# Optimization experiments

Hardware: AMD Instinct MI355X
Metric: run time of the kernel (lower is better)

Reference implementation:

```python
import jax, jax.numpy as jnp
import numpy as np

NUM_HEADS = 8
KEY_DIM = 512      # total projected dim across heads
VALUE_DIM = 512
EMBED_DIM = 512


def setup_inputs() -> dict:
    key = jax.random.key(0)
    ks = jax.random.split(key, 12)
    B, S, E = 8, 1024, EMBED_DIM
    sc_in = 1.0 / np.sqrt(E)
    sc_o = 1.0 / np.sqrt(KEY_DIM)
    return {
        "queries": jax.random.normal(ks[0], (B, S, E), jnp.float32),
        "keys": jax.random.normal(ks[1], (B, S, E), jnp.float32),
        "values": jax.random.normal(ks[2], (B, S, E), jnp.float32),
        "Wq": jax.random.normal(ks[3], (E, KEY_DIM), jnp.float32) * sc_in,
        "bq": jnp.zeros((KEY_DIM,), jnp.float32),
        "Wk": jax.random.normal(ks[4], (E, KEY_DIM), jnp.float32) * sc_in,
        "bk": jnp.zeros((KEY_DIM,), jnp.float32),
        "Wv": jax.random.normal(ks[5], (E, VALUE_DIM), jnp.float32) * sc_in,
        "bv": jnp.zeros((VALUE_DIM,), jnp.float32),
        "Wo": jax.random.normal(ks[6], (KEY_DIM, EMBED_DIM), jnp.float32) * sc_o,
        "bo": jnp.zeros((EMBED_DIM,), jnp.float32),
    }


def _split_heads(x):
    # [B, S, key_dim] -> [B, H, S, key_dim//H]
    B, S, D = x.shape
    return x.reshape(B, S, NUM_HEADS, D // NUM_HEADS).transpose(0, 2, 1, 3)


def reference(queries, keys, values, Wq, bq, Wk, bk, Wv, bv, Wo, bo):
    q = _split_heads(queries @ Wq + bq)   # [B,H,S,dh]
    k = _split_heads(keys @ Wk + bk)
    v = _split_heads(values @ Wv + bv)
    # NOTE: original scales by sqrt(full key_dim), not per-head dim
    scores = jnp.einsum("bhqd,bhkd->bhqk", q, k) / jnp.sqrt(
        jnp.asarray(KEY_DIM, jnp.float32))
    weights = jax.nn.softmax(scores, axis=-1)
    o = jnp.einsum("bhqk,bhkd->bhqd", weights, v)  # [B,H,S,dh]
    B, H, S, dh = o.shape
    o = o.transpose(0, 2, 1, 3).reshape(B, S, H * dh)  # merge heads -> key_dim
    return o @ Wo + bo
```

## Files before the change

### kernel.cpp

```cpp
#include <hip/hip_runtime.h>


typedef __bf16 bf16x8 __attribute__((ext_vector_type(8)));
typedef __bf16 bf16x4 __attribute__((ext_vector_type(4)));
typedef float  f32x4  __attribute__((ext_vector_type(4)));

#define MFMA(a, b, c) __builtin_amdgcn_mfma_f32_16x16x32_bf16((a), (b), (c), 0, 0, 0)

__device__ inline bf16x8 cvt8(const float* p) {
  f32x4 u = *(const f32x4*)p;
  f32x4 v = *(const f32x4*)(p + 4);
  bf16x8 r;
  r[0] = (__bf16)u[0]; r[1] = (__bf16)u[1]; r[2] = (__bf16)u[2]; r[3] = (__bf16)u[3];
  r[4] = (__bf16)v[0]; r[5] = (__bf16)v[1]; r[6] = (__bf16)v[2]; r[7] = (__bf16)v[3];
  return r;
}

__device__ inline void gl_lds(const __bf16* g, __bf16* l) {
  __builtin_amdgcn_global_load_lds((const __attribute__((address_space(1))) void*)g,
                                   (__attribute__((address_space(3))) void*)l, 16, 0, 0);
}

__global__ __launch_bounds__(256) void cvt_qkv(const float* __restrict__ Q,
                                               const float* __restrict__ K,
                                               const float* __restrict__ V,
                                               __bf16* __restrict__ Qo,
                                               __bf16* __restrict__ Ko,
                                               __bf16* __restrict__ Vo) {
  const float* src;
  __bf16* dst;
  switch (blockIdx.y) {
    case 0: src = Q; dst = Qo; break;
    case 1: src = K; dst = Ko; break;
    default: src = V; dst = Vo; break;
  }
  const long idx = ((long)blockIdx.x * 256 + threadIdx.x) * 8;
  *(bf16x8*)(dst + idx) = cvt8(src + idx);
}

__global__ __launch_bounds__(256) void transpose_w4(const float* __restrict__ W0,
                                                    const float* __restrict__ W1,
                                                    const float* __restrict__ W2,
                                                    const float* __restrict__ W3,
                                                    __bf16* __restrict__ O0,
                                                    __bf16* __restrict__ O1,
                                                    __bf16* __restrict__ O2,
                                                    __bf16* __restrict__ O3,
                                                    float s0) {
  const float* in;
  __bf16* out;
  float sc = 1.0f;
  switch (blockIdx.y) {
    case 0: in = W0; out = O0; sc = s0; break;
    case 1: in = W1; out = O1; break;
    case 2: in = W2; out = O2; break;
    default: in = W3; out = O3; break;
  }
  __shared__ __align__(16) float t[64][65];
  const int tk = (blockIdx.x & 7) * 64;
  const int tn = (blockIdx.x >> 3) * 64;
  const int r0 = threadIdx.x >> 4;
  const int c4 = threadIdx.x & 15;
#pragma unroll
  for (int i = 0; i < 4; ++i) {
    int r = r0 + i * 16;
    f32x4 v = *(const f32x4*)(in + (long)(tk + r) * 512 + tn + c4 * 4);
#pragma unroll
    for (int j = 0; j < 4; ++j) t[r][c4 * 4 + j] = v[j] * sc;
  }
  __syncthreads();
  const int n0 = threadIdx.x >> 3;
  const int k8 = threadIdx.x & 7;
#pragma unroll
  for (int i = 0; i < 2; ++i) {
    int n = n0 + i * 32;
    bf16x8 v;
#pragma unroll
    for (int j = 0; j < 8; ++j) v[j] = (__bf16)t[k8 * 8 + j][n];
    *(bf16x8*)(out + (long)(tn + n) * 512 + tk + k8 * 8) = v;
  }
}

template <int MODE, typename OT>
__device__ __forceinline__ void gemm_core(const __bf16* __restrict__ X,
                                          const __bf16* __restrict__ Wt,
                                          const float* __restrict__ bias,
                                          OT* __restrict__ out, float bsc,
                                          char* smem) {
  __bf16 (*At)[4096] = (__bf16(*)[4096])smem;
  __bf16 (*Bt)[4096] = (__bf16(*)[4096])(smem + 16384);

  const int tid = threadIdx.x;
  const int lane = tid & 63, wid = tid >> 6, quad = lane >> 4, l16 = lane & 15;
  const int i = blockIdx.x;
  const int kk = i >> 3;
  const int bm = ((i & 7) * 8 + (kk >> 2)) * 128;
  const int bn = (kk & 3) * 128;
  const int wm = (wid >> 1) * 64;
  const int wn = (wid & 1) * 64;

  f32x4 acc[4][4] = {};

  const int rowB = lane >> 2;
  const int gB = (lane & 3) ^ ((rowB >> 1) & 3);

#define STAGE(bi, k0)                                                          \
  {                                                                            \
    _Pragma("unroll") for (int j = 0; j < 2; ++j) {                            \
      const int g = wid * 2 + j;                       \
      gl_lds(X + (long)(bm + g * 16 + rowB) * 512 + (k0) + (gB << 3),          \
             &At[bi][g * 512 + lane * 8]);                                     \
      gl_lds(Wt + (long)(bn + g * 16 + rowB) * 512 + (k0) + (gB << 3),         \
             &Bt[bi][g * 512 + lane * 8]);                                     \
    }                                                                          \
  }

  STAGE(0, 0);

  const int posm = quad ^ ((l16 >> 1) & 3);
  for (int c = 0; c < 16; ++c) {
    const int bi = c & 1;
    __syncthreads();
    if (c < 15) STAGE(bi ^ 1, (c + 1) * 32);

    bf16x8 a[4], b[4];
#pragma unroll
    for (int t = 0; t < 4; ++t) {
      a[t] = *(const bf16x8*)(&At[bi][(wm + t * 16 + l16) * 32 + (posm << 3)]);
      b[t] = *(const bf16x8*)(&Bt[bi][(wn + t * 16 + l16) * 32 + (posm << 3)]);
    }
#pragma unroll
    for (int mt = 0; mt < 4; ++mt)
#pragma unroll
      for (int nt = 0; nt < 4; ++nt) acc[mt][nt] = MFMA(a[mt], b[nt], acc[mt][nt]);
  }
#undef STAGE

  if constexpr (MODE == 4) {
    __syncthreads();
    __bf16* tb = (__bf16*)smem;
#pragma unroll
    for (int nt = 0; nt < 4; ++nt) {
      const int n = wn + nt * 16 + l16;
      const float bvv = bias[bn + n] * bsc;
#pragma unroll
      for (int mt = 0; mt < 4; ++mt) {
        const int m0 = wm + mt * 16 + quad * 4;
        bf16x4 w;
#pragma unroll
        for (int r = 0; r < 4; ++r) w[r] = (__bf16)(acc[mt][nt][r] + bvv);
        *(bf16x4*)(&tb[n * 128 + (((m0 >> 3) ^ (n & 15)) << 3) + (m0 & 7)]) = w;
      }
    }
    __syncthreads();
    const int nn = tid & 127, mhalf = tid >> 7;
    const int d = nn & 63, h = (bn + nn) >> 6;
    const int bb = bm >> 10;
    OT* ob = out + (long)(bb * 8 + h) * 65536;
#pragma unroll
    for (int gi = 0; gi < 8; ++gi) {
      const int gl = mhalf * 8 + gi;
      bf16x8 v = *(const bf16x8*)(&tb[nn * 128 + ((gl ^ (nn & 15)) << 3)]);
      const int cidx = ((bm & 1023) + (gl << 3)) >> 6;
      *(bf16x8*)(ob + cidx * 4096 + d * 64 + ((gi ^ (d & 7)) << 3)) = v;
    }
    return;
  }

#pragma unroll
  for (int nt = 0; nt < 4; ++nt) {
    const int n = bn + wn + nt * 16 + l16;
    const float bvv = bias[n] * bsc;
    const int h = n >> 6, d = n & 63;
#pragma unroll
    for (int mt = 0; mt < 4; ++mt) {
#pragma unroll
      for (int r = 0; r < 4; ++r) {
        const int m = bm + wm + mt * 16 + quad * 4 + r;
        const float v = acc[mt][nt][r] + bvv;
        if constexpr (MODE == 0) {
          out[(long)m * 512 + n] = (OT)v;
        } else if constexpr (MODE == 1) {
          const int bb = m >> 10, s = m & 1023;
          out[((long)((bb * 8 + h) * 1024 + s)) * 64 + d] = (OT)v;
        } else {
          const int bb = m >> 10, s = m & 1023;
          const long idx = (long)(bb * 8 + h) * 65536 + (s >> 6) * 4096 +
                           (s & 63) * 64 + (((d >> 3) ^ (s & 7)) << 3) + (d & 7);
          out[idx] = (OT)v;
        }
      }
    }
  }
}

__global__ __launch_bounds__(256) void gemm_qkv(
    const __bf16* __restrict__ Qx, const __bf16* __restrict__ Kx,
    const __bf16* __restrict__ Vx, const __bf16* __restrict__ Wqt,
    const __bf16* __restrict__ Wkt, const __bf16* __restrict__ Wvt,
    const float* __restrict__ bq, const float* __restrict__ bk,
    const float* __restrict__ bv, __bf16* __restrict__ Qp,
    __bf16* __restrict__ Kp, __bf16* __restrict__ Vtp, float qscale) {
  __shared__ __align__(16) char smem[32768];
  if (blockIdx.y == 0)
    gemm_core<1, __bf16>(Qx, Wqt, bq, Qp, qscale, smem);
  else if (blockIdx.y == 1)
    gemm_core<3, __bf16>(Kx, Wkt, bk, Kp, 1.0f, smem);
  else
    gemm_core<4, __bf16>(Vx, Wvt, bv, Vtp, 1.0f, smem);
}

__global__ __launch_bounds__(256) void gemm_o(const __bf16* __restrict__ Oc,
                                              const __bf16* __restrict__ Wot,
                                              const float* __restrict__ bo,
                                              float* __restrict__ out) {
  __shared__ __align__(16) char smem[32768];
  gemm_core<0, float>(Oc, Wot, bo, out, 1.0f, smem);
}

__global__ __launch_bounds__(256) void attn(const __bf16* __restrict__ Q,
                                            const __bf16* __restrict__ K,
                                            const __bf16* __restrict__ Vt,
                                            __bf16* __restrict__ Oc) {
  __shared__ __align__(16) __bf16 kbuf[2][4096];
  __shared__ __align__(16) __bf16 vbuf[2][4096];
  __shared__ __align__(16) __bf16 plds[4][32 * 64];

  const int tid = threadIdx.x;
  const int lane = tid & 63, wid = tid >> 6, quad = lane >> 4, l16 = lane & 15;
  const int i = blockIdx.x;
  const int pair = (i & 7) + (((i >> 6) & 7) << 3);
  const int qt = (i >> 3) & 7;
  const int q0 = qt * 128 + wid * 32;
  const int b = pair >> 3, h = pair & 7;
  const int swz = l16 & 7;

  const __bf16* Qb = Q + (long)pair * 65536;
  const __bf16* Kb = K + (long)pair * 65536;
  const __bf16* Vb = Vt + (long)pair * 65536;
  __bf16* pw = plds[wid];

  bf16x8 bq[2][2];
#pragma unroll
  for (int t = 0; t < 2; ++t)
#pragma unroll
    for (int e = 0; e < 2; ++e)
      bq[t][e] = *(const bf16x8*)(Qb + (q0 + t * 16 + l16) * 64 + e * 32 + quad * 8);

  float lr[2] = {0.f, 0.f};
  f32x4 oa[2][4] = {};

  {
    const __bf16* kg = Kb + tid * 8;
    const __bf16* vg = Vb + tid * 8;
    gl_lds(kg, &kbuf[0][tid * 8]);
    gl_lds(kg + 2048, &kbuf[0][2048 + tid * 8]);
    gl_lds(vg, &vbuf[0][tid * 8]);
    gl_lds(vg + 2048, &vbuf[0][2048 + tid * 8]);
  }

  for (int c = 0; c < 16; ++c) {
    const int bi = c & 1;
    __syncthreads();
    if (c < 15) {
      const __bf16* kg = Kb + (c + 1) * 4096 + tid * 8;
      const __bf16* vg = Vb + (c + 1) * 4096 + tid * 8;
      gl_lds(kg, &kbuf[bi ^ 1][tid * 8]);
      gl_lds(kg + 2048, &kbuf[bi ^ 1][2048 + tid * 8]);
      gl_lds(vg, &vbuf[bi ^ 1][tid * 8]);
      gl_lds(vg + 2048, &vbuf[bi ^ 1][2048 + tid * 8]);
    }

    f32x4 s[2][4] = {};
#pragma unroll
    for (int kt = 0; kt < 4; ++kt) {
      const int krow = (kt * 16 + l16) * 64;
      bf16x8 a0 = *(const bf16x8*)(&kbuf[bi][krow + ((quad ^ swz) << 3)]);
      bf16x8 a1 = *(const bf16x8*)(&kbuf[bi][krow + (((4 + quad) ^ swz) << 3)]);
#pragma unroll
      for (int t = 0; t < 2; ++t) {
        s[t][kt] = MFMA(a0, bq[t][0], s[t][kt]);
        s[t][kt] = MFMA(a1, bq[t][1], s[t][kt]);
      }
    }

#pragma unroll
    for (int t = 0; t < 2; ++t) {
      const int prow = (t * 16 + l16) * 64;
#pragma unroll
      for (int kt = 0; kt < 4; ++kt) {
        bf16x4 w;
#pragma unroll
        for (int r = 0; r < 4; ++r) {
          const float p = __expf(s[t][kt][r]);
          lr[t] += p;
          w[r] = (__bf16)p;
        }
        *(bf16x4*)(&pw[prow + (((kt * 2 + (quad >> 1)) ^ swz) << 3) + (quad & 1) * 4]) = w;
      }
    }
    bf16x8 pb[2][2];
#pragma unroll
    for (int t = 0; t < 2; ++t)
#pragma unroll
      for (int e = 0; e < 2; ++e)
        pb[t][e] = *(const bf16x8*)(&pw[(t * 16 + l16) * 64 + (((e * 4 + quad) ^ swz) << 3)]);

#pragma unroll
    for (int nt = 0; nt < 4; ++nt) {
      const int drow = (nt * 16 + l16) * 64;
      bf16x8 v0 = *(const bf16x8*)(&vbuf[bi][drow + ((quad ^ swz) << 3)]);
      bf16x8 v1 = *(const bf16x8*)(&vbuf[bi][drow + (((4 + quad) ^ swz) << 3)]);
#pragma unroll
      for (int t = 0; t < 2; ++t) {
        oa[t][nt] = MFMA(v0, pb[t][0], oa[t][nt]);
        oa[t][nt] = MFMA(v1, pb[t][1], oa[t][nt]);
      }
    }
  }

#pragma unroll
  for (int t = 0; t < 2; ++t) {
    lr[t] += __shfl_xor(lr[t], 16);
    lr[t] += __shfl_xor(lr[t], 32);
    const float inv = 1.0f / lr[t];
    const long base = ((long)b * 1024 + q0 + t * 16 + l16) * 512 + h * 64 + quad * 4;
#pragma unroll
    for (int nt = 0; nt < 4; ++nt) {
      bf16x4 w;
#pragma unroll
      for (int r = 0; r < 4; ++r) w[r] = (__bf16)(oa[t][nt][r] * inv);
      *(bf16x4*)(Oc + base + nt * 16) = w;
    }
  }
}

extern "C" void kernel_launch(void* const* d_in, const int* in_sizes, int n_in,
                              void* d_out, int out_size, void* d_ws, size_t ws_size,
                              hipStream_t stream) {
  const float* queries = (const float*)d_in[0];
  const float* keys = (const float*)d_in[1];
  const float* values = (const float*)d_in[2];
  const float* Wq = (const float*)d_in[3];
  const float* bq = (const float*)d_in[4];
  const float* Wk = (const float*)d_in[5];
  const float* bk = (const float*)d_in[6];
  const float* Wv = (const float*)d_in[7];
  const float* bv = (const float*)d_in[8];
  const float* Wo = (const float*)d_in[9];
  const float* bo = (const float*)d_in[10];
  float* out = (float*)d_out;

  __bf16* ws = (__bf16*)d_ws;
  const long WSZ = 512 * 512;
  const long XSZ = 8192L * 512;
  __bf16* Wqt = ws;
  __bf16* Wkt = ws + WSZ;
  __bf16* Wvt = ws + 2 * WSZ;
  __bf16* Wot = ws + 3 * WSZ;
  __bf16* Qp = ws + 4 * WSZ;
  __bf16* Kp = Qp + XSZ;
  __bf16* Vtp = Kp + XSZ;
  __bf16* Oc = Vtp + XSZ;
  __bf16* Qbf = Oc + XSZ;
  __bf16* Kbf = Qbf + XSZ;
  __bf16* Vbf = Kbf + XSZ;

  const float qscale = 0.04419417382415922f;

  cvt_qkv<<<dim3(2048, 3), 256, 0, stream>>>(queries, keys, values, Qbf, Kbf, Vbf);
  transpose_w4<<<dim3(64, 4), 256, 0, stream>>>(Wq, Wk, Wv, Wo, Wqt, Wkt, Wvt, Wot,
                                                qscale);

  gemm_qkv<<<dim3(256, 3), 256, 0, stream>>>(Qbf, Kbf, Vbf, Wqt, Wkt, Wvt,
                                             bq, bk, bv, Qp, Kp, Vtp, qscale);

  attn<<<512, 256, 0, stream>>>(Qp, Kp, Vtp, Oc);

  gemm_o<<<256, 256, 0, stream>>>(Oc, Wot, bo, out);
}
```

Baseline: 176.3 us.

## Fuse fp32-to-bf16 input conversion into QKV GEMM and use exp2 softmax

Removes the separate cvt_qkv kernel. The QKV GEMM now loads fp32 activations into registers, converts them to bf16 and writes them into LDS after the MFMA step, so the pipeline stays double-buffered. This saves one kernel launch and a full write and re-read of bf16 copies of Q/K/V, at the cost of doubled global read bytes per tile, more registers, and register-staged rather than direct-to-LDS loads. It also folds log2(e) into the query scale so the softmax can use exp2f instead of __expf.

After: 184.4 us. +4.6%, slower.

```diff
diff --git a/kernel.cpp b/kernel.cpp
--- a/kernel.cpp
+++ b/kernel.cpp
@@ -7,9 +7,7 @@
 
 #define MFMA(a, b, c) __builtin_amdgcn_mfma_f32_16x16x32_bf16((a), (b), (c), 0, 0, 0)
 
-__device__ inline bf16x8 cvt8(const float* p) {
-  f32x4 u = *(const f32x4*)p;
-  f32x4 v = *(const f32x4*)(p + 4);
+__device__ inline bf16x8 cvt8r(f32x4 u, f32x4 v) {
   bf16x8 r;
   r[0] = (__bf16)u[0]; r[1] = (__bf16)u[1]; r[2] = (__bf16)u[2]; r[3] = (__bf16)u[3];
   r[4] = (__bf16)v[0]; r[5] = (__bf16)v[1]; r[6] = (__bf16)v[2]; r[7] = (__bf16)v[3];
@@ -19,23 +17,6 @@
 __device__ inline void gl_lds(const __bf16* g, __bf16* l) {
   __builtin_amdgcn_global_load_lds((const __attribute__((address_space(1))) void*)g,
                                    (__attribute__((address_space(3))) void*)l, 16, 0, 0);
-}
-
-__global__ __launch_bounds__(256) void cvt_qkv(const float* __restrict__ Q,
-                                               const float* __restrict__ K,
-                                               const float* __restrict__ V,
-                                               __bf16* __restrict__ Qo,
-                                               __bf16* __restrict__ Ko,
-                                               __bf16* __restrict__ Vo) {
-  const float* src;
-  __bf16* dst;
-  switch (blockIdx.y) {
-    case 0: src = Q; dst = Qo; break;
-    case 1: src = K; dst = Ko; break;
-    default: src = V; dst = Vo; break;
-  }
-  const long idx = ((long)blockIdx.x * 256 + threadIdx.x) * 8;
-  *(bf16x8*)(dst + idx) = cvt8(src + idx);
 }
 
 __global__ __launch_bounds__(256) void transpose_w4(const float* __restrict__ W0,
@@ -81,12 +62,13 @@
   }
 }
 
-template <int MODE, typename OT>
-__device__ __forceinline__ void gemm_core(const __bf16* __restrict__ X,
+template <int MODE, typename OT, typename XT>
+__device__ __forceinline__ void gemm_core(const XT* __restrict__ X,
                                           const __bf16* __restrict__ Wt,
                                           const float* __restrict__ bias,
                                           OT* __restrict__ out, float bsc,
                                           char* smem) {
+  constexpr bool F32X = (sizeof(XT) == 4);
   __bf16 (*At)[4096] = (__bf16(*)[4096])smem;
   __bf16 (*Bt)[4096] = (__bf16(*)[4096])(smem + 16384);
 
@@ -104,24 +86,67 @@
   const int rowB = lane >> 2;
   const int gB = (lane & 3) ^ ((rowB >> 1) & 3);
 
-#define STAGE(bi, k0)                                                          \
+  const long xoff = (long)(bm + rowB) * 512 + (gB << 3);
+  const long woff = (long)(bn + rowB) * 512 + (gB << 3);
+
+  f32x4 xr[2][2];
+
+#define STAGE_W(bi, k0)                                                        \
   {                                                                            \
     _Pragma("unroll") for (int j = 0; j < 2; ++j) {                            \
       const int g = wid * 2 + j;                       \
-      gl_lds(X + (long)(bm + g * 16 + rowB) * 512 + (k0) + (gB << 3),          \
+      gl_lds(Wt + woff + (long)g * 16 * 512 + (k0), &Bt[bi][g * 512 + lane * 8]); \
+    }                                                                          \
+  }
+
+#define STAGE_X_LDS(bi, k0)                                                    \
+  {                                                                            \
+    _Pragma("unroll") for (int j = 0; j < 2; ++j) {                            \
+      const int g = wid * 2 + j;                                               \
+      gl_lds((const __bf16*)X + xoff + (long)g * 16 * 512 + (k0),              \
              &At[bi][g * 512 + lane * 8]);                                     \
-      gl_lds(Wt + (long)(bn + g * 16 + rowB) * 512 + (k0) + (gB << 3),         \
-             &Bt[bi][g * 512 + lane * 8]);                                     \
     }                                                                          \
   }
 
-  STAGE(0, 0);
+#define XLOAD(k0)                                                              \
+  {                                                                            \
+    _Pragma("unroll") for (int j = 0; j < 2; ++j) {                            \
+      const int g = wid * 2 + j;                                               \
+      const float* sp = (const float*)X + xoff + (long)g * 16 * 512 + (k0);    \
+      xr[j][0] = *(const f32x4*)sp;                                            \
+      xr[j][1] = *(const f32x4*)(sp + 4);                                      \
+    }                                                                          \
+  }
+
+#define XWRITE(bi)                                                             \
+  {                                                                            \
+    _Pragma("unroll") for (int j = 0; j < 2; ++j) {                            \
+      const int g = wid * 2 + j;                                               \
+      *(bf16x8*)(&At[(bi)][g * 512 + lane * 8]) = cvt8r(xr[j][0], xr[j][1]);   \
+    }                                                                          \
+  }
+
+  if constexpr (F32X) {
+    XLOAD(0);
+    STAGE_W(0, 0);
+    XWRITE(0);
+  } else {
+    STAGE_X_LDS(0, 0);
+    STAGE_W(0, 0);
+  }
 
   const int posm = quad ^ ((l16 >> 1) & 3);
   for (int c = 0; c < 16; ++c) {
     const int bi = c & 1;
     __syncthreads();
-    if (c < 15) STAGE(bi ^ 1, (c + 1) * 32);
+    if (c < 15) {
+      if constexpr (F32X) {
+        XLOAD((c + 1) * 32);
+      } else {
+        STAGE_X_LDS(bi ^ 1, (c + 1) * 32);
+      }
+      STAGE_W(bi ^ 1, (c + 1) * 32);
+    }
 
     bf16x8 a[4], b[4];
 #pragma unroll
@@ -133,8 +158,15 @@
     for (int mt = 0; mt < 4; ++mt)
 #pragma unroll
       for (int nt = 0; nt < 4; ++nt) acc[mt][nt] = MFMA(a[mt], b[nt], acc[mt][nt]);
-  }
-#undef STAGE
+
+    if constexpr (F32X) {
+      if (c < 15) XWRITE(bi ^ 1);
+    }
+  }
+#undef STAGE_W
+#undef STAGE_X_LDS
+#undef XLOAD
+#undef XWRITE
 
   if constexpr (MODE == 4) {
     __syncthreads();
@@ -195,19 +227,19 @@
 }
 
 __global__ __launch_bounds__(256) void gemm_qkv(
-    const __bf16* __restrict__ Qx, const __bf16* __restrict__ Kx,
-    const __bf16* __restrict__ Vx, const __bf16* __restrict__ Wqt,
+    const float* __restrict__ Qx, const float* __restrict__ Kx,
+    const float* __restrict__ Vx, const __bf16* __restrict__ Wqt,
     const __bf16* __restrict__ Wkt, const __bf16* __restrict__ Wvt,
     const float* __restrict__ bq, const float* __restrict__ bk,
     const float* __restrict__ bv, __bf16* __restrict__ Qp,
     __bf16* __restrict__ Kp, __bf16* __restrict__ Vtp, float qscale) {
   __shared__ __align__(16) char smem[32768];
   if (blockIdx.y == 0)
-    gemm_core<1, __bf16>(Qx, Wqt, bq, Qp, qscale, smem);
+    gemm_core<1, __bf16, float>(Qx, Wqt, bq, Qp, qscale, smem);
   else if (blockIdx.y == 1)
-    gemm_core<3, __bf16>(Kx, Wkt, bk, Kp, 1.0f, smem);
+    gemm_core<3, __bf16, float>(Kx, Wkt, bk, Kp, 1.0f, smem);
   else
-    gemm_core<4, __bf16>(Vx, Wvt, bv, Vtp, 1.0f, smem);
+    gemm_core<4, __bf16, float>(Vx, Wvt, bv, Vtp, 1.0f, smem);
 }
 
 __global__ __launch_bounds__(256) void gemm_o(const __bf16* __restrict__ Oc,
@@ -215,7 +247,7 @@
                                               const float* __restrict__ bo,
                                               float* __restrict__ out) {
   __shared__ __align__(16) char smem[32768];
-  gemm_core<0, float>(Oc, Wot, bo, out, 1.0f, smem);
+  gemm_core<0, float, __bf16>(Oc, Wot, bo, out, 1.0f, smem);
 }
 
 __global__ __launch_bounds__(256) void attn(const __bf16* __restrict__ Q,
@@ -292,7 +324,7 @@
         bf16x4 w;
 #pragma unroll
         for (int r = 0; r < 4; ++r) {
-          const float p = __expf(s[t][kt][r]);
+          const float p = exp2f(s[t][kt][r]);
           lr[t] += p;
           w[r] = (__bf16)p;
         }
@@ -362,17 +394,13 @@
   __bf16* Kp = Qp + XSZ;
   __bf16* Vtp = Kp + XSZ;
   __bf16* Oc = Vtp + XSZ;
-  __bf16* Qbf = Oc + XSZ;
-  __bf16* Kbf = Qbf + XSZ;
-  __bf16* Vbf = Kbf + XSZ;
-
-  const float qscale = 0.04419417382415922f;
-
-  cvt_qkv<<<dim3(2048, 3), 256, 0, stream>>>(queries, keys, values, Qbf, Kbf, Vbf);
+
+  const float qscale = 0.044194173824159216f * 1.4426950408889634f;
+
   transpose_w4<<<dim3(64, 4), 256, 0, stream>>>(Wq, Wk, Wv, Wo, Wqt, Wkt, Wvt, Wot,
                                                 qscale);
 
-  gemm_qkv<<<dim3(256, 3), 256, 0, stream>>>(Qbf, Kbf, Vbf, Wqt, Wkt, Wvt,
+  gemm_qkv<<<dim3(256, 3), 256, 0, stream>>>(queries, keys, values, Wqt, Wkt, Wvt,
                                              bq, bk, bv, Qp, Kp, Vtp, qscale);
 
   attn<<<512, 256, 0, stream>>>(Qp, Kp, Vtp, Oc);
```

## Triple-buffer LDS staging with explicit vmcnt waits and fold log2e into Q scale

Applied to the files above, without the earlier changes.

Both GEMM and attention kernels move from double to triple buffering of global-to-LDS loads. Each iteration waits with an explicit s_waitcnt vmcnt(4) plus s_barrier, so loads issued two chunks ahead stay in flight while the current chunk computes. The softmax now uses exp2f, with log2(e) folded into the query scale applied at projection time. LDS use grows to 48KB per GEMM block and more for attention, which may lower occupancy. The hand-counted vmcnt values also depend on the exact number of loads issued per stage.

Measured after the change: 181.6 us. 3.0% more time.

```diff
diff --git a/kernel.cpp b/kernel.cpp
--- a/kernel.cpp
+++ b/kernel.cpp
@@ -6,6 +6,8 @@
 typedef float  f32x4  __attribute__((ext_vector_type(4)));
 
 #define MFMA(a, b, c) __builtin_amdgcn_mfma_f32_16x16x32_bf16((a), (b), (c), 0, 0, 0)
+
+#define WAITN_BAR(N) asm volatile("s_waitcnt vmcnt(" #N ")\n\ts_barrier" ::: "memory")
 
 __device__ inline bf16x8 cvt8(const float* p) {
   f32x4 u = *(const f32x4*)p;
@@ -87,8 +89,8 @@
                                           const float* __restrict__ bias,
                                           OT* __restrict__ out, float bsc,
                                           char* smem) {
-  __bf16 (*At)[4096] = (__bf16(*)[4096])smem;
-  __bf16 (*Bt)[4096] = (__bf16(*)[4096])(smem + 16384);
+  __bf16* At = (__bf16*)smem;
+  __bf16* Bt = (__bf16*)(smem + 24576);
 
   const int tid = threadIdx.x;
   const int lane = tid & 63, wid = tid >> 6, quad = lane >> 4, l16 = lane & 15;
@@ -104,37 +106,46 @@
   const int rowB = lane >> 2;
   const int gB = (lane & 3) ^ ((rowB >> 1) & 3);
 
-#define STAGE(bi, k0)                                                          \
-  {                                                                            \
-    _Pragma("unroll") for (int j = 0; j < 2; ++j) {                            \
-      const int g = wid * 2 + j;                       \
-      gl_lds(X + (long)(bm + g * 16 + rowB) * 512 + (k0) + (gB << 3),          \
-             &At[bi][g * 512 + lane * 8]);                                     \
-      gl_lds(Wt + (long)(bn + g * 16 + rowB) * 512 + (k0) + (gB << 3),         \
-             &Bt[bi][g * 512 + lane * 8]);                                     \
-    }                                                                          \
-  }
-
-  STAGE(0, 0);
+  auto stage = [&](int off, int k0) {
+#pragma unroll
+    for (int j = 0; j < 2; ++j) {
+      const int g = wid * 2 + j;
+      gl_lds(X + (long)(bm + g * 16 + rowB) * 512 + k0 + (gB << 3),
+             &At[off + g * 512 + lane * 8]);
+      gl_lds(Wt + (long)(bn + g * 16 + rowB) * 512 + k0 + (gB << 3),
+             &Bt[off + g * 512 + lane * 8]);
+    }
+  };
 
   const int posm = quad ^ ((l16 >> 1) & 3);
-  for (int c = 0; c < 16; ++c) {
-    const int bi = c & 1;
-    __syncthreads();
-    if (c < 15) STAGE(bi ^ 1, (c + 1) * 32);
-
+
+  auto compute = [&](int co) {
     bf16x8 a[4], b[4];
 #pragma unroll
     for (int t = 0; t < 4; ++t) {
-      a[t] = *(const bf16x8*)(&At[bi][(wm + t * 16 + l16) * 32 + (posm << 3)]);
-      b[t] = *(const bf16x8*)(&Bt[bi][(wn + t * 16 + l16) * 32 + (posm << 3)]);
+      a[t] = *(const bf16x8*)(&At[co + (wm + t * 16 + l16) * 32 + (posm << 3)]);
+      b[t] = *(const bf16x8*)(&Bt[co + (wn + t * 16 + l16) * 32 + (posm << 3)]);
     }
 #pragma unroll
     for (int mt = 0; mt < 4; ++mt)
 #pragma unroll
       for (int nt = 0; nt < 4; ++nt) acc[mt][nt] = MFMA(a[mt], b[nt], acc[mt][nt]);
-  }
-#undef STAGE
+  };
+
+  stage(0, 0);
+  stage(4096, 32);
+
+  int co = 0, so = 8192;
+  for (int c = 0; c < 15; ++c) {
+    WAITN_BAR(4);
+    if (c < 14) stage(so, (c + 2) * 32);
+    compute(co);
+    const int nc = 12288 - co - so;
+    so = co;
+    co = nc;
+  }
+  WAITN_BAR(0);
+  compute(co);
 
   if constexpr (MODE == 4) {
     __syncthreads();
@@ -201,7 +212,7 @@
     const float* __restrict__ bq, const float* __restrict__ bk,
     const float* __restrict__ bv, __bf16* __restrict__ Qp,
     __bf16* __restrict__ Kp, __bf16* __restrict__ Vtp, float qscale) {
-  __shared__ __align__(16) char smem[32768];
+  __shared__ __align__(16) char smem[49152];
   if (blockIdx.y == 0)
     gemm_core<1, __bf16>(Qx, Wqt, bq, Qp, qscale, smem);
   else if (blockIdx.y == 1)
@@ -214,7 +225,7 @@
                                               const __bf16* __restrict__ Wot,
                                               const float* __restrict__ bo,
                                               float* __restrict__ out) {
-  __shared__ __align__(16) char smem[32768];
+  __shared__ __align__(16) char smem[49152];
   gemm_core<0, float>(Oc, Wot, bo, out, 1.0f, smem);
 }
 
@@ -222,9 +233,9 @@
                                             const __bf16* __restrict__ K,
                                             const __bf16* __restrict__ Vt,
                                             __bf16* __restrict__ Oc) {
-  __shared__ __align__(16) __bf16 kbuf[2][4096];
-  __shared__ __align__(16) __bf16 vbuf[2][4096];
-  __shared__ __align__(16) __bf16 plds[4][32 * 64];
+  __shared__ __align__(16) __bf16 kbuf[12288];
+  __shared__ __align__(16) __bf16 vbuf[12288];
+  __shared__ __align__(16) __bf16 plds[4][2048];
 
   const int tid = threadIdx.x;
   const int lane = tid & 63, wid = tid >> 6, quad = lane >> 4, l16 = lane & 15;
@@ -246,37 +257,27 @@
 #pragma unroll
     for (int e = 0; e < 2; ++e)
       bq[t][e] = *(const bf16x8*)(Qb + (q0 + t * 16 + l16) * 64 + e * 32 + quad * 8);
+  asm volatile("s_waitcnt vmcnt(0)" ::: "memory");
 
   float lr[2] = {0.f, 0.f};
   f32x4 oa[2][4] = {};
 
-  {
-    const __bf16* kg = Kb + tid * 8;
-    const __bf16* vg = Vb + tid * 8;
-    gl_lds(kg, &kbuf[0][tid * 8]);
-    gl_lds(kg + 2048, &kbuf[0][2048 + tid * 8]);
-    gl_lds(vg, &vbuf[0][tid * 8]);
-    gl_lds(vg + 2048, &vbuf[0][2048 + tid * 8]);
-  }
-
-  for (int c = 0; c < 16; ++c) {
-    const int bi = c & 1;
-    __syncthreads();
-    if (c < 15) {
-      const __bf16* kg = Kb + (c + 1) * 4096 + tid * 8;
-      const __bf16* vg = Vb + (c + 1) * 4096 + tid * 8;
-      gl_lds(kg, &kbuf[bi ^ 1][tid * 8]);
-      gl_lds(kg + 2048, &kbuf[bi ^ 1][2048 + tid * 8]);
-      gl_lds(vg, &vbuf[bi ^ 1][tid * 8]);
-      gl_lds(vg + 2048, &vbuf[bi ^ 1][2048 + tid * 8]);
-    }
-
+  auto stage = [&](int off, int c_) {
+    const __bf16* kg = Kb + c_ * 4096 + tid * 8;
+    const __bf16* vg = Vb + c_ * 4096 + tid * 8;
+    gl_lds(kg, &kbuf[off + tid * 8]);
+    gl_lds(kg + 2048, &kbuf[off + 2048 + tid * 8]);
+    gl_lds(vg, &vbuf[off + tid * 8]);
+    gl_lds(vg + 2048, &vbuf[off + 2048 + tid * 8]);
+  };
+
+  auto body = [&](int co) {
     f32x4 s[2][4] = {};
 #pragma unroll
     for (int kt = 0; kt < 4; ++kt) {
-      const int krow = (kt * 16 + l16) * 64;
-      bf16x8 a0 = *(const bf16x8*)(&kbuf[bi][krow + ((quad ^ swz) << 3)]);
-      bf16x8 a1 = *(const bf16x8*)(&kbuf[bi][krow + (((4 + quad) ^ swz) << 3)]);
+      const int krow = co + (kt * 16 + l16) * 64;
+      bf16x8 a0 = *(const bf16x8*)(&kbuf[krow + ((quad ^ swz) << 3)]);
+      bf16x8 a1 = *(const bf16x8*)(&kbuf[krow + (((4 + quad) ^ swz) << 3)]);
 #pragma unroll
       for (int t = 0; t < 2; ++t) {
         s[t][kt] = MFMA(a0, bq[t][0], s[t][kt]);
@@ -292,7 +293,7 @@
         bf16x4 w;
 #pragma unroll
         for (int r = 0; r < 4; ++r) {
-          const float p = __expf(s[t][kt][r]);
+          const float p = exp2f(s[t][kt][r]);
           lr[t] += p;
           w[r] = (__bf16)p;
         }
@@ -308,16 +309,31 @@
 
 #pragma unroll
     for (int nt = 0; nt < 4; ++nt) {
-      const int drow = (nt * 16 + l16) * 64;
-      bf16x8 v0 = *(const bf16x8*)(&vbuf[bi][drow + ((quad ^ swz) << 3)]);
-      bf16x8 v1 = *(const bf16x8*)(&vbuf[bi][drow + (((4 + quad) ^ swz) << 3)]);
+      const int drow = co + (nt * 16 + l16) * 64;
+      bf16x8 v0 = *(const bf16x8*)(&vbuf[drow + ((quad ^ swz) << 3)]);
+      bf16x8 v1 = *(const bf16x8*)(&vbuf[drow + (((4 + quad) ^ swz) << 3)]);
 #pragma unroll
       for (int t = 0; t < 2; ++t) {
         oa[t][nt] = MFMA(v0, pb[t][0], oa[t][nt]);
         oa[t][nt] = MFMA(v1, pb[t][1], oa[t][nt]);
       }
     }
-  }
+  };
+
+  stage(0, 0);
+  stage(4096, 1);
+
+  int co = 0, so = 8192;
+  for (int c = 0; c < 15; ++c) {
+    WAITN_BAR(4);
+    if (c < 14) stage(so, c + 2);
+    body(co);
+    const int nc = 12288 - co - so;
+    so = co;
+    co = nc;
+  }
+  WAITN_BAR(0);
+  body(co);
 
 #pragma unroll
   for (int t = 0; t < 2; ++t) {
@@ -366,7 +382,7 @@
   __bf16* Kbf = Qbf + XSZ;
   __bf16* Vbf = Kbf + XSZ;
 
-  const float qscale = 0.04419417382415922f;
+  const float qscale = 0.044194173824159216f * 1.4426950408889634f;
 
   cvt_qkv<<<dim3(2048, 3), 256, 0, stream>>>(queries, keys, values, Qbf, Kbf, Vbf);
   transpose_w4<<<dim3(64, 4), 256, 0, stream>>>(Wq, Wk, Wv, Wo, Wqt, Wkt, Wvt, Wot,
```
